# Kernel tuning notes

Measured on AMD Instinct MI355X. Metric: run time of the kernel, lower is better.

Reference implementation:

```python
import jax, jax.numpy as jnp
import numpy as np

B, C_IN, C_OUT, RED, H, W = 8, 256, 64, 16, 256, 256
K = 3


def setup_inputs() -> dict:
    key = jax.random.key(0)
    k1, k2, k3, k4, k5 = jax.random.split(key, 5)
    x = jax.random.normal(k1, (B, C_OUT, H, W), dtype=jnp.float32)
    vec = jax.random.normal(k2, (B, C_IN), dtype=jnp.float32)
    # ChanNorm affine params
    g = jnp.ones((1, C_OUT, 1, 1), dtype=jnp.float32)
    b = jnp.zeros((1, C_OUT, 1, 1), dtype=jnp.float32)
    # conv_du MLP (torch Linear weights: [out, in], no bias)
    w1 = jax.random.normal(k3, (C_IN // RED, C_IN), dtype=jnp.float32) / np.sqrt(C_IN)
    w2 = jax.random.normal(k4, (C_OUT, C_IN // RED), dtype=jnp.float32) / np.sqrt(C_IN // RED)
    # Conv2DMod weight, kaiming normal fan_in (leaky_relu a=0): std=sqrt(2/fan_in)
    fan_in = C_OUT * K * K
    wconv = jax.random.normal(k5, (C_OUT, C_OUT, K, K), dtype=jnp.float32) * np.sqrt(2.0 / fan_in)
    return {"x": x, "vec": vec, "g": g, "b": b, "w1": w1, "w2": w2, "wconv": wconv}


def reference(x, vec, g, b, w1, w2, wconv):
    eps_norm = 1e-5
    eps_mod = 1e-8
    # ChanNorm: normalize over channel dim (unbiased=False var)
    mean = jnp.mean(x, axis=1, keepdims=True)
    var = jnp.mean((x - mean) ** 2, axis=1, keepdims=True)
    nx = (x - mean) / jnp.sqrt(var + eps_norm) * g + b
    # style MLP: Linear -> LeakyReLU(0.1) -> Linear (no biases)
    hid = jax.nn.leaky_relu(vec @ w1.T, negative_slope=0.1)
    sty = hid @ w2.T  # [B, C_OUT]
    # per-sample modulated weights: [B, O, I, K, K]
    weights = wconv[None, :, :, :, :] * (sty[:, None, :, None, None] + 1.0)
    # demodulate
    d = jax.lax.rsqrt(jnp.sum(weights ** 2, axis=(2, 3, 4), keepdims=True) + eps_mod)
    weights = weights * d
    # grouped conv with groups=B == per-sample conv; same padding for k=3,s=1,d=1 -> 1
    pad = ((H - 1) * 0 + 1 * (K - 1)) // 2
    def per_sample_conv(xi, wi):
        # xi: [C,H,W], wi: [O,I,K,K]
        return jax.lax.conv_general_dilated(
            xi[None], wi, window_strides=(1, 1),
            padding=[(pad, pad), (pad, pad)],
            dimension_numbers=("NCHW", "OIHW", "NCHW"))[0]
    out = jax.vmap(per_sample_conv)(nx, weights)  # [B, O, H, W]
    return out + x
```

## Files before the change

### kernel.cpp

```cpp
#include <hip/hip_runtime.h>
#include <hip/hip_bf16.h>

typedef __hip_bfloat16 bf16;
typedef __attribute__((ext_vector_type(8))) short short8;
typedef __attribute__((ext_vector_type(4))) float float4v;

#define Hd 256
#define Wd 256
#define HW 65536
#define CO 64

__global__ __launch_bounds__(64) void k1_style(
    const float* __restrict__ vec, const float* __restrict__ w1,
    const float* __restrict__ w2, const float* __restrict__ wconv,
    bf16* __restrict__ wA)
{
    int o = blockIdx.x;
    int s = blockIdx.y;
    int i = threadIdx.x;

    float sv[4];
#pragma unroll
    for (int q = 0; q < 4; ++q) sv[q] = vec[s * 256 + q * 64 + i];

    float hid[16];
#pragma unroll
    for (int j = 0; j < 16; ++j) {
        float p = 0.f;
#pragma unroll
        for (int q = 0; q < 4; ++q) p += sv[q] * w1[j * 256 + q * 64 + i];
#pragma unroll
        for (int off = 32; off >= 1; off >>= 1) p += __shfl_xor(p, off, 64);
        hid[j] = p > 0.f ? p : 0.1f * p;
    }
    float sty = 0.f;
#pragma unroll
    for (int j = 0; j < 16; ++j) sty += w2[i * 16 + j] * hid[j];
    float msty = sty + 1.0f;

    float wrow[9];
#pragma unroll
    for (int tt = 0; tt < 9; ++tt) wrow[tt] = wconv[(o * 64 + i) * 9 + tt] * msty;
    float ss = 0.f;
#pragma unroll
    for (int tt = 0; tt < 9; ++tt) ss += wrow[tt] * wrow[tt];
#pragma unroll
    for (int off = 32; off >= 1; off >>= 1) ss += __shfl_xor(ss, off, 64);
    float d = rsqrtf(ss + 1e-8f);

    bf16* wAs = wA + s * (18 * 64 * 32);
#pragma unroll
    for (int tt = 0; tt < 9; ++tt) {
        int k = tt * 64 + i;
        wAs[(k >> 5) * 2048 + o * 32 + (k & 31)] = (bf16)(wrow[tt] * d);
    }
}

__global__ __launch_bounds__(256) void k2_norm(
    const float* __restrict__ x, const float* __restrict__ gg,
    const float* __restrict__ bb, bf16* __restrict__ nx,
    float2* __restrict__ sms)
{
    int bx = blockIdx.x;
    int h  = bx >> 2, qx = (bx & 3) * 64;
    int s  = blockIdx.y;
    int t  = threadIdx.x;
    int cg = t & 15;
    int pg = t >> 4;
    int px = qx + pg * 4;
    float4 g4 = *(const float4*)&gg[cg * 4];
    float4 b4 = *(const float4*)&bb[cg * 4];
    const float* xrow = x + (size_t)s * ((size_t)CO * HW) + (size_t)h * Wd;
    bf16*   nxrow  = nx  + ((size_t)s * HW + (size_t)h * Wd) * CO;
    float2* smsrow = sms +  (size_t)s * HW + (size_t)h * Wd;

    float4 v[4];
#pragma unroll
    for (int cc = 0; cc < 4; ++cc)
        v[cc] = *(const float4*)&xrow[(size_t)(cg * 4 + cc) * HW + px];

    float s1[4], s2[4];
#pragma unroll
    for (int pi = 0; pi < 4; ++pi) {
        float a0 = (&v[0].x)[pi], a1 = (&v[1].x)[pi];
        float a2 = (&v[2].x)[pi], a3 = (&v[3].x)[pi];
        s1[pi] = (a0 + a1) + (a2 + a3);
        s2[pi] = (a0 * a0 + a1 * a1) + (a2 * a2 + a3 * a3);
    }
#pragma unroll
    for (int off = 1; off <= 8; off <<= 1)
#pragma unroll
        for (int pi = 0; pi < 4; ++pi) {
            s1[pi] += __shfl_xor(s1[pi], off, 64);
            s2[pi] += __shfl_xor(s2[pi], off, 64);
        }
    float mean[4], rstd[4];
#pragma unroll
    for (int pi = 0; pi < 4; ++pi) {
        mean[pi] = s1[pi] * (1.f / 64);
        float var = s2[pi] * (1.f / 64) - mean[pi] * mean[pi];
        rstd[pi] = rsqrtf(var + 1e-5f);
    }
    if (cg == 0) {
#pragma unroll
        for (int pi = 0; pi < 4; ++pi)
            smsrow[px + pi] = make_float2(mean[pi], sqrtf(s2[pi] * (1.f / 64) - mean[pi] * mean[pi] + 1e-5f));
    }
#pragma unroll
    for (int pi = 0; pi < 4; ++pi) {
        union { uint2 u; bf16 hh[4]; } o;
#pragma unroll
        for (int cc = 0; cc < 4; ++cc) {
            float f  = (&v[cc].x)[pi];
            float gv = (&g4.x)[cc], bv = (&b4.x)[cc];
            o.hh[cc] = (bf16)((f - mean[pi]) * rstd[pi] * gv + bv);
        }
        *(uint2*)&nxrow[(size_t)(px + pi) * CO + cg * 4] = o.u;
    }
}

#define PXB 32
#define ROWS 8
#define TR 10
#define WL 34
#define NSITES (TR * WL)
#define ROW_ELEMS (8 * WL * 8)

union U4 { uint4 u; bf16 h[8]; short8 s8; };

__global__ __launch_bounds__(256) void k3_conv(
    const bf16* __restrict__ nx, const float2* __restrict__ sms,
    const float* __restrict__ gg, const float* __restrict__ bb,
    const bf16* __restrict__ wA, float* __restrict__ out)
{
    int w0 = blockIdx.x * PXB;
    int h0 = blockIdx.y * ROWS;
    int s  = blockIdx.z;
    int t  = threadIdx.x;
    __shared__ __align__(16) bf16 tile[TR * ROW_ELEMS];
    __shared__ float2 sbi[64];
    if (t < 64) sbi[t] = make_float2(bb[t], 1.0f / gg[t]);

    int p0 = t, p1 = t + 256;
    bool live1 = (p1 < NSITES);
    int dr0 = p0 / WL, wl0 = p0 - dr0 * WL;
    int dr1 = live1 ? (p1 / WL) : 0;
    int wl1 = live1 ? (p1 - dr1 * WL) : 0;
    int grow0 = h0 + dr0 - 1, wab0 = w0 + wl0 - 1;
    int grow1 = h0 + dr1 - 1, wab1 = w0 + wl1 - 1;
    bool ok0 = (grow0 >= 0 && grow0 < Hd && wab0 >= 0 && wab0 < Wd);
    bool ok1 = live1 && (grow1 >= 0 && grow1 < Hd && wab1 >= 0 && wab1 < Wd);
    const bf16* np0 = nx + ((size_t)s * HW + (size_t)grow0 * Wd + wab0) * CO;
    const bf16* np1 = nx + ((size_t)s * HW + (size_t)grow1 * Wd + wab1) * CO;
    bf16* dst0 = &tile[dr0 * ROW_ELEMS + wl0 * 8];
    bf16* dst1 = &tile[dr1 * ROW_ELEMS + wl1 * 8];
    uint4 z = make_uint4(0u, 0u, 0u, 0u);
#pragma unroll
    for (int c8 = 0; c8 < 8; ++c8) {
        uint4 a = ok0 ? *(const uint4*)&np0[c8 * 8] : z;
        *(uint4*)&dst0[c8 * (WL * 8)] = a;
    }
    if (live1) {
#pragma unroll
        for (int c8 = 0; c8 < 8; ++c8) {
            uint4 a = ok1 ? *(const uint4*)&np1[c8 * 8] : z;
            *(uint4*)&dst1[c8 * (WL * 8)] = a;
        }
    }

    int wave = t >> 6, lane = t & 63;
    int mi = wave & 1, ni = wave >> 1;
    int col = lane & 15, quad = lane >> 4;

    const bf16* wAs = wA + s * (18 * 64 * 32);
    const bf16* pa0 = wAs + (mi * 32 + col) * 32 + quad * 8;
    const bf16* pa1 = wAs + (mi * 32 + 16 + col) * 32 + quad * 8;
    U4 a0c, a1c;
    a0c.u = *(const uint4*)pa0;
    a1c.u = *(const uint4*)pa1;

    int wpx = w0 + ni * 16 + col;
    float2 msr[ROWS];
#pragma unroll
    for (int r = 0; r < ROWS; ++r)
        msr[r] = sms[(size_t)s * HW + (size_t)(h0 + r) * Wd + wpx];

    __syncthreads();

    float4v acc[2][ROWS];
#pragma unroll
    for (int mt = 0; mt < 2; ++mt)
#pragma unroll
        for (int r = 0; r < ROWS; ++r) acc[mt][r] = (float4v)0.f;

    int base = ni * 16 + col;
#pragma unroll 1
    for (int kc = 0; kc < 18; ++kc) {
        U4 a0n, a1n;
        a0n.u = *(const uint4*)(pa0 + (kc + 1) * 2048);
        a1n.u = *(const uint4*)(pa1 + (kc + 1) * 2048);
        int tap = kc >> 1;
        int kh = (tap * 11) >> 5;
        int kw = tap - kh * 3;
        int ch8 = (kc & 1) * 4 + quad;
        const bf16* bp = &tile[kh * ROW_ELEMS + (ch8 * WL + base + kw) * 8];
#pragma unroll
        for (int r = 0; r < ROWS; ++r) {
            U4 b; b.u = *(const uint4*)&bp[r * ROW_ELEMS];
            acc[0][r] = __builtin_amdgcn_mfma_f32_16x16x32_bf16(a0c.s8, b.s8, acc[0][r], 0, 0, 0);
            acc[1][r] = __builtin_amdgcn_mfma_f32_16x16x32_bf16(a1c.s8, b.s8, acc[1][r], 0, 0, 0);
        }
        a0c = a0n; a1c = a1n;
    }

    int wl_i = base + 1;
#pragma unroll
    for (int r = 0; r < ROWS; ++r) {
        int grow = h0 + r;
        float2 ms = msr[r];
#pragma unroll
        for (int mt = 0; mt < 2; ++mt) {
#pragma unroll
            for (int rr = 0; rr < 4; ++rr) {
                int o = mi * 32 + mt * 16 + quad * 4 + rr;
                float nxf = __bfloat162float(
                    tile[(r + 1) * ROW_ELEMS + ((o >> 3) * WL + wl_i) * 8 + (o & 7)]);
                float2 bi = sbi[o];
                float xrec = (nxf - bi.x) * bi.y * ms.y + ms.x;
                size_t idx = (size_t)(s * CO + o) * HW + (size_t)grow * Wd + wpx;
                out[idx] = acc[mt][r][rr] + xrec;
            }
        }
    }
}

extern "C" void kernel_launch(void* const* d_in, const int* in_sizes, int n_in,
                              void* d_out, int out_size, void* d_ws, size_t ws_size,
                              hipStream_t stream)
{
    const float* x     = (const float*)d_in[0];
    const float* vec   = (const float*)d_in[1];
    const float* g     = (const float*)d_in[2];
    const float* bb    = (const float*)d_in[3];
    const float* w1    = (const float*)d_in[4];
    const float* w2    = (const float*)d_in[5];
    const float* wconv = (const float*)d_in[6];
    float* out = (float*)d_out;

    char* wsb = (char*)d_ws;
    bf16*   wA  = (bf16*)wsb;
    bf16*   nx  = (bf16*)(wsb + ((size_t)1 << 20));
    float2* sms = (float2*)(wsb + ((size_t)65 << 20));

    k1_style<<<dim3(64, 8), 64, 0, stream>>>(vec, w1, w2, wconv, wA);
    k2_norm<<<dim3(1024, 8), 256, 0, stream>>>(x, g, bb, nx, sms);
    k3_conv<<<dim3(8, 32, 8), 256, 0, stream>>>(nx, sms, g, bb, wA, out);
}
```

Before: 324.9 us.

## Restage norm output through LDS for coalesced stores; vectorize conv epilogue reads

The norm kernel now has each wave cover 32 pixels with 8 channels per lane. It writes the normalized bf16 values into a shared buffer and copies them out with fully coalesced 16-byte stores, replacing scattered 8-byte stores. The grid is halved to match. The conv epilogue now hoists the per-channel bias/scale into registers and reads the four nx values with one 8-byte LDS load instead of four scalar loads. The norm kernel gains an LDS buffer and a barrier, and each thread holds more registers.

```diff
diff --git a/kernel.cpp b/kernel.cpp
--- a/kernel.cpp
+++ b/kernel.cpp
@@ -61,34 +61,35 @@
     const float* __restrict__ bb, bf16* __restrict__ nx,
     float2* __restrict__ sms)
 {
-    int bx = blockIdx.x;
-    int h  = bx >> 2, qx = (bx & 3) * 64;
-    int s  = blockIdx.y;
-    int t  = threadIdx.x;
-    int cg = t & 15;
-    int pg = t >> 4;
-    int px = qx + pg * 4;
-    float4 g4 = *(const float4*)&gg[cg * 4];
-    float4 b4 = *(const float4*)&bb[cg * 4];
+    int bx  = blockIdx.x;
+    int h   = bx >> 1;
+    int seg = (bx & 1) * 128;
+    int s   = blockIdx.y;
+    int t   = threadIdx.x;
+    int wave = t >> 6, lane = t & 63;
+    int po = lane & 7;
+    int cg = lane >> 3;
+
+    __shared__ __align__(16) char lbuf[4][4096];
+
+    int pxw = seg + wave * 32;
     const float* xrow = x + (size_t)s * ((size_t)CO * HW) + (size_t)h * Wd;
-    bf16*   nxrow  = nx  + ((size_t)s * HW + (size_t)h * Wd) * CO;
-    float2* smsrow = sms +  (size_t)s * HW + (size_t)h * Wd;
-
-    float4 v[4];
-#pragma unroll
-    for (int cc = 0; cc < 4; ++cc)
-        v[cc] = *(const float4*)&xrow[(size_t)(cg * 4 + cc) * HW + px];
+
+    float4 v[8];
+#pragma unroll
+    for (int c = 0; c < 8; ++c)
+        v[c] = *(const float4*)&xrow[(size_t)(cg * 8 + c) * HW + pxw + po * 4];
 
     float s1[4], s2[4];
 #pragma unroll
     for (int pi = 0; pi < 4; ++pi) {
-        float a0 = (&v[0].x)[pi], a1 = (&v[1].x)[pi];
-        float a2 = (&v[2].x)[pi], a3 = (&v[3].x)[pi];
-        s1[pi] = (a0 + a1) + (a2 + a3);
-        s2[pi] = (a0 * a0 + a1 * a1) + (a2 * a2 + a3 * a3);
-    }
-#pragma unroll
-    for (int off = 1; off <= 8; off <<= 1)
+        float a = 0.f, q = 0.f;
+#pragma unroll
+        for (int c = 0; c < 8; ++c) { float f = (&v[c].x)[pi]; a += f; q += f * f; }
+        s1[pi] = a; s2[pi] = q;
+    }
+#pragma unroll
+    for (int off = 8; off <= 32; off <<= 1)
 #pragma unroll
         for (int pi = 0; pi < 4; ++pi) {
             s1[pi] += __shfl_xor(s1[pi], off, 64);
@@ -98,24 +99,38 @@
 #pragma unroll
     for (int pi = 0; pi < 4; ++pi) {
         mean[pi] = s1[pi] * (1.f / 64);
-        float var = s2[pi] * (1.f / 64) - mean[pi] * mean[pi];
-        rstd[pi] = rsqrtf(var + 1e-5f);
+        float var = s2[pi] * (1.f / 64) - mean[pi] * mean[pi] + 1e-5f;
+        rstd[pi] = rsqrtf(var);
     }
     if (cg == 0) {
-#pragma unroll
-        for (int pi = 0; pi < 4; ++pi)
-            smsrow[px + pi] = make_float2(mean[pi], sqrtf(s2[pi] * (1.f / 64) - mean[pi] * mean[pi] + 1e-5f));
-    }
+        float2* smsrow = sms + (size_t)s * HW + (size_t)h * Wd;
+#pragma unroll
+        for (int pi = 0; pi < 4; ++pi) {
+            float var = s2[pi] * (1.f / 64) - mean[pi] * mean[pi] + 1e-5f;
+            smsrow[pxw + po * 4 + pi] = make_float2(mean[pi], var * rstd[pi]);
+        }
+    }
+
+    float4 gA = *(const float4*)&gg[cg * 8], gB = *(const float4*)&gg[cg * 8 + 4];
+    float4 bA = *(const float4*)&bb[cg * 8], bB = *(const float4*)&bb[cg * 8 + 4];
 #pragma unroll
     for (int pi = 0; pi < 4; ++pi) {
-        union { uint2 u; bf16 hh[4]; } o;
-#pragma unroll
-        for (int cc = 0; cc < 4; ++cc) {
-            float f  = (&v[cc].x)[pi];
-            float gv = (&g4.x)[cc], bv = (&b4.x)[cc];
-            o.hh[cc] = (bf16)((f - mean[pi]) * rstd[pi] * gv + bv);
-        }
-        *(uint2*)&nxrow[(size_t)(px + pi) * CO + cg * 4] = o.u;
+        union { uint4 u; bf16 hh[8]; } ov;
+#pragma unroll
+        for (int c = 0; c < 8; ++c) {
+            float gv = (c < 4) ? (&gA.x)[c] : (&gB.x)[c - 4];
+            float bv = (c < 4) ? (&bA.x)[c] : (&bB.x)[c - 4];
+            ov.hh[c] = (bf16)(((&v[c].x)[pi] - mean[pi]) * rstd[pi] * gv + bv);
+        }
+        int p = po * 4 + pi;
+        *(uint4*)&lbuf[wave][(size_t)p * 128 + cg * 16] = ov.u;
+    }
+    __syncthreads();
+    bf16* nxw = nx + ((size_t)s * HW + (size_t)h * Wd + pxw) * CO;
+#pragma unroll
+    for (int i = 0; i < 4; ++i) {
+        uint4 d = *(uint4*)&lbuf[wave][i * 1024 + lane * 16];
+        *(uint4*)((char*)nxw + i * 1024 + lane * 16) = d;
     }
 }
 
@@ -187,6 +202,13 @@
 
     __syncthreads();
 
+    float2 bi8[2][4];
+#pragma unroll
+    for (int mt = 0; mt < 2; ++mt)
+#pragma unroll
+        for (int rr = 0; rr < 4; ++rr)
+            bi8[mt][rr] = sbi[mi * 32 + mt * 16 + quad * 4 + rr];
+
     float4v acc[2][ROWS];
 #pragma unroll
     for (int mt = 0; mt < 2; ++mt)
@@ -220,15 +242,16 @@
         float2 ms = msr[r];
 #pragma unroll
         for (int mt = 0; mt < 2; ++mt) {
+            int o0 = mi * 32 + mt * 16 + quad * 4;
+            int c8o = o0 >> 3;
+            union { uint2 u; bf16 hh[4]; } nv;
+            nv.u = *(const uint2*)&tile[(r + 1) * ROW_ELEMS + (c8o * WL + wl_i) * 8 + (o0 & 7)];
+            size_t idx0 = (size_t)(s * CO + o0) * HW + (size_t)grow * Wd + wpx;
 #pragma unroll
             for (int rr = 0; rr < 4; ++rr) {
-                int o = mi * 32 + mt * 16 + quad * 4 + rr;
-                float nxf = __bfloat162float(
-                    tile[(r + 1) * ROW_ELEMS + ((o >> 3) * WL + wl_i) * 8 + (o & 7)]);
-                float2 bi = sbi[o];
-                float xrec = (nxf - bi.x) * bi.y * ms.y + ms.x;
-                size_t idx = (size_t)(s * CO + o) * HW + (size_t)grow * Wd + wpx;
-                out[idx] = acc[mt][r][rr] + xrec;
+                float2 bi = bi8[mt][rr];
+                float xrec = (__bfloat162float(nv.hh[rr]) - bi.x) * bi.y * ms.y + ms.x;
+                out[idx0 + (size_t)rr * HW] = acc[mt][r][rr] + xrec;
             }
         }
     }
@@ -253,6 +276,6 @@
     float2* sms = (float2*)(wsb + ((size_t)65 << 20));
 
     k1_style<<<dim3(64, 8), 64, 0, stream>>>(vec, w1, w2, wconv, wA);
-    k2_norm<<<dim3(1024, 8), 256, 0, stream>>>(x, g, bb, nx, sms);
+    k2_norm<<<dim3(512, 8), 256, 0, stream>>>(x, g, bb, nx, sms);
     k3_conv<<<dim3(8, 32, 8), 256, 0, stream>>>(nx, sms, g, bb, wA, out);
 }
```

After: 329.6 us. About the same (+1.5%).
